# Performance work log

Hardware: AMD Instinct MI355X
Metric: run time of the kernel (lower is better)

Reference implementation:

```python
import jax, jax.numpy as jnp
import numpy as np

B, D, H, W = 16, 96, 96, 96
NUM_POINTS = 4096
THRESH = 0.5
CH = [3, 64, 128, 256, 512]   # shared-MLP channel progression (3 mlp layers + global_dim)
GROUPS = 8
EPS = 1e-5
HEAD_HIDDEN = 128


def setup_inputs() -> dict:
    key = jax.random.key(0)
    ks = jax.random.split(key, 8)
    inp = {"volume": jax.random.uniform(ks[0], (B, 1, D, H, W), jnp.float32)}
    for i in range(4):
        # Conv1d(kernel=1, no bias) weight (out, in); kaiming normal fan_out -> std=sqrt(2/out)
        inp[f"w{i+1}"] = jax.random.normal(ks[1 + i], (CH[i + 1], CH[i]), jnp.float32) * np.sqrt(2.0 / CH[i + 1]).astype(np.float32)
        inp[f"gn{i+1}_w"] = jnp.ones((CH[i + 1],), jnp.float32)
        inp[f"gn{i+1}_b"] = jnp.zeros((CH[i + 1],), jnp.float32)
    inp["fc1_w"] = jax.random.normal(ks[5], (HEAD_HIDDEN, CH[-1]), jnp.float32) * np.sqrt(2.0 / HEAD_HIDDEN).astype(np.float32)
    inp["fc1_b"] = jnp.zeros((HEAD_HIDDEN,), jnp.float32)
    inp["fc2_w"] = jax.random.normal(ks[6], (1, HEAD_HIDDEN), jnp.float32) * np.sqrt(2.0).astype(np.float32)
    inp["fc2_b"] = jnp.zeros((1,), jnp.float32)
    return inp


def volume_to_points(volume):
    """Batched, jit-safe version of volume_to_pointcloud (eval mode: linspace sampling)."""
    b, _, d, h, w = volume.shape
    mask = (volume[:, 0] > THRESH).reshape(b, -1)              # (B, D*H*W)
    n = mask.sum(axis=1)                                        # (B,) foreground counts
    # Stable argsort on ~mask puts foreground flat-indices first, in ascending order
    # == torch nonzero() ordering (row-major over D,H,W).
    order = jnp.argsort(jnp.logical_not(mask), axis=1, stable=True)  # (B, D*H*W)
    p = jnp.arange(NUM_POINTS)
    n_f = n.astype(jnp.float32)[:, None]
    # torch.linspace(0, n-1, P).long(): truncation toward zero
    lin = (p[None, :].astype(jnp.float32) * (n_f - 1.0) / (NUM_POINTS - 1)).astype(jnp.int32)
    lin = jnp.clip(lin, 0, jnp.maximum(n[:, None] - 1, 0))
    wrap = p[None, :] % jnp.maximum(n[:, None], 1)              # n < P fallback
    idx = jnp.where(n[:, None] >= NUM_POINTS, lin, wrap)        # (B, P)
    flat = jnp.take_along_axis(order, idx, axis=1)              # (B, P) flat voxel indices
    dd = flat // (h * w)
    hh = (flat // w) % h
    ww = flat % w
    coords = jnp.stack([dd, hh, ww], axis=1).astype(jnp.float32)  # (B, 3, P)
    scale = jnp.array([max(d - 1, 1), max(h - 1, 1), max(w - 1, 1)], jnp.float32)
    pts = coords / scale[None, :, None] * 2.0 - 1.0
    return jnp.where((n > 0)[:, None, None], pts, 0.0)


def group_norm(x, gamma, beta):
    b, c, npts = x.shape
    xg = x.reshape(b, GROUPS, c // GROUPS, npts)
    mu = xg.mean(axis=(2, 3), keepdims=True)
    var = xg.var(axis=(2, 3), keepdims=True)
    xn = ((xg - mu) * jax.lax.rsqrt(var + EPS)).reshape(b, c, npts)
    return xn * gamma[None, :, None] + beta[None, :, None]


def reference(volume, w1, gn1_w, gn1_b, w2, gn2_w, gn2_b, w3, gn3_w, gn3_b,
              w4, gn4_w, gn4_b, fc1_w, fc1_b, fc2_w, fc2_b):
    x = volume_to_points(volume)                                 # (B, 3, P)
    for cw, gw, gb in ((w1, gn1_w, gn1_b), (w2, gn2_w, gn2_b),
                       (w3, gn3_w, gn3_b), (w4, gn4_w, gn4_b)):
        x = jax.nn.relu(group_norm(jnp.einsum('oc,bcn->bon', cw, x), gw, gb))
    g = x.max(axis=2)                                            # (B, 512) global max-pool
    hdn = jax.nn.relu(g @ fc1_w.T + fc1_b)                       # dropout is identity in eval
    logits = (hdn @ fc2_w.T + fc2_b)[:, 0]                       # squeeze(-1) -> (B,)
    return logits
```

## Files before the change

### kernel.cpp

```cpp
#include <hip/hip_runtime.h>
#include <hip/hip_bf16.h>

#define NB 16
#define VOX 884736
#define NPTS 4096
#define CHUNK 1024
#define NCHUNK 864

typedef _Float16 f16x8 __attribute__((ext_vector_type(8)));
typedef _Float16 f16x4 __attribute__((ext_vector_type(4)));
typedef float f32x4 __attribute__((ext_vector_type(4)));


__global__ __launch_bounds__(256) void count_kernel(const float* __restrict__ vol,
                                                    int* __restrict__ counts,
                                                    unsigned long long* __restrict__ bits) {
    int blk = blockIdx.x;
    const float4* v4 = (const float4*)(vol + (size_t)blk * CHUNK);
    float4 v = v4[threadIdx.x];
    int nib = (v.x > 0.5f) | ((v.y > 0.5f) << 1) | ((v.z > 0.5f) << 2) | ((v.w > 0.5f) << 3);
    __shared__ unsigned char nibs[256];
    nibs[threadIdx.x] = (unsigned char)nib;
    int cnt = __popc(nib);
    for (int off = 32; off; off >>= 1) cnt += __shfl_down(cnt, off, 64);
    __shared__ int s[4];
    if ((threadIdx.x & 63) == 0) s[threadIdx.x >> 6] = cnt;
    __syncthreads();
    if (threadIdx.x < 16) {
        unsigned long long wd = 0;
        #pragma unroll
        for (int i = 0; i < 16; i++)
            wd |= (unsigned long long)nibs[threadIdx.x * 16 + i] << (4 * i);
        bits[(size_t)blk * 16 + threadIdx.x] = wd;
    }
    if (threadIdx.x == 0) counts[blk] = s[0] + s[1] + s[2] + s[3];
}

__global__ __launch_bounds__(1024) void scan_kernel(const int* __restrict__ counts,
                                                    int* __restrict__ prefix,
                                                    int* __restrict__ totals) {
    __shared__ int s[1024];
    int b = blockIdx.x, t = threadIdx.x;
    int v = (t < NCHUNK) ? counts[b * NCHUNK + t] : 0;
    s[t] = v;
    __syncthreads();
    for (int off = 1; off < 1024; off <<= 1) {
        int x = (t >= off) ? s[t - off] : 0;
        __syncthreads();
        s[t] += x;
        __syncthreads();
    }
    if (t < NCHUNK) prefix[b * NCHUNK + t] = s[t] - v;
    if (t == NCHUNK - 1) totals[b] = s[t];
}


__global__ __launch_bounds__(256) void points_kernel(const unsigned long long* __restrict__ bits,
                                                     const int* __restrict__ prefix,
                                                     const int* __restrict__ totals,
                                                     const float* __restrict__ w1,
                                                     float* __restrict__ pts,
                                                     float* __restrict__ pstat1) {
    int b = blockIdx.x >> 4;
    int pc = blockIdx.x & 15;
    int p = pc * 256 + threadIdx.x;
    __shared__ int spref[NCHUNK];
    __shared__ float sw1[192];
    for (int i = threadIdx.x; i < NCHUNK; i += 256) spref[i] = prefix[b * NCHUNK + i];
    if (threadIdx.x < 192) sw1[threadIdx.x] = w1[threadIdx.x];
    __syncthreads();
    int n = totals[b];
    float px = 0.f, py = 0.f, pz = 0.f;
    if (n > 0) {
        int k;
        if (n >= NPTS) {
            float t = (float)p * ((float)n - 1.0f);
            t = t / 4095.0f;
            k = (int)t;
            if (k > n - 1) k = n - 1;
            if (k < 0) k = 0;
        } else {
            k = p % n;
        }
        int lo = 0, hi = NCHUNK - 1;
        while (lo < hi) {
            int mid = (lo + hi + 1) >> 1;
            if (spref[mid] <= k) lo = mid; else hi = mid - 1;
        }
        int rr = k - spref[lo];
        const unsigned long long* wb = bits + ((size_t)b * NCHUNK + lo) * 16;
        unsigned long long chosen = 0;
        int wordidx = 0;
        bool found = false;
        #pragma unroll
        for (int w = 0; w < 16; w++) {
            unsigned long long m = wb[w];
            int pcnt = __popcll(m);
            bool take = (!found) && (rr < pcnt);
            if (take) { chosen = m; wordidx = w; found = true; }
            if (!found) rr -= pcnt;
        }
        int pos = 0;
        unsigned long long m64 = chosen;
        int c = __popcll(m64 & 0xFFFFFFFFull);
        if (rr >= c) { pos = 32; rr -= c; m64 >>= 32; }
        unsigned mm = (unsigned)m64;
        c = __popc(mm & 0xFFFFu); if (rr >= c) { pos += 16; rr -= c; mm >>= 16; }
        c = __popc(mm & 0xFFu);   if (rr >= c) { pos += 8;  rr -= c; mm >>= 8; }
        c = __popc(mm & 0xFu);    if (rr >= c) { pos += 4;  rr -= c; mm >>= 4; }
        c = __popc(mm & 0x3u);    if (rr >= c) { pos += 2;  rr -= c; mm >>= 2; }
        c = mm & 1u;              if (rr >= c) { pos += 1; }
        int flat = lo * CHUNK + wordidx * 64 + pos;
        int dd = flat / 9216;
        int rem = flat - dd * 9216;
        int hh = rem / 96;
        int ww = rem - hh * 96;
        px = (float)dd / 95.0f * 2.0f - 1.0f;
        py = (float)hh / 95.0f * 2.0f - 1.0f;
        pz = (float)ww / 95.0f * 2.0f - 1.0f;
    }
    pts[((size_t)b * 3 + 0) * NPTS + p] = px;
    pts[((size_t)b * 3 + 1) * NPTS + p] = py;
    pts[((size_t)b * 3 + 2) * NPTS + p] = pz;
    float s[8] = {}, q[8] = {};
    #pragma unroll
    for (int o = 0; o < 64; o++) {
        float a = sw1[o * 3 + 0] * px + sw1[o * 3 + 1] * py + sw1[o * 3 + 2] * pz;
        s[o >> 3] += a;
        q[o >> 3] += a * a;
    }
    __shared__ float red[4][8][2];
    int wv = threadIdx.x >> 6;
    #pragma unroll
    for (int g = 0; g < 8; g++) {
        float S = s[g], Q = q[g];
        for (int off = 32; off; off >>= 1) {
            S += __shfl_down(S, off, 64);
            Q += __shfl_down(Q, off, 64);
        }
        if ((threadIdx.x & 63) == 0) { red[wv][g][0] = S; red[wv][g][1] = Q; }
    }
    __syncthreads();
    if (threadIdx.x < 8) {
        int g = threadIdx.x;
        float S = red[0][g][0] + red[1][g][0] + red[2][g][0] + red[3][g][0];
        float Q = red[0][g][1] + red[1][g][1] + red[2][g][1] + red[3][g][1];
        float* d = pstat1 + (((size_t)(b * 8 + g)) * 16 + pc) * 2;
        d[0] = S; d[1] = Q;
    }
}

__global__ __launch_bounds__(64) void gn_finalize1(const float* __restrict__ pstat,
                                                   const float* __restrict__ gamma,
                                                   const float* __restrict__ beta,
                                                   float* __restrict__ scale,
                                                   float* __restrict__ shift) {
    int b = blockIdx.x >> 3, g = blockIdx.x & 7;
    const float* base = pstat + (size_t)(b * 8 + g) * 32;
    float S = 0.f, Q = 0.f;
    if (threadIdx.x < 16) { S = base[threadIdx.x * 2]; Q = base[threadIdx.x * 2 + 1]; }
    for (int off = 8; off; off >>= 1) {
        S += __shfl_down(S, off, 64);
        Q += __shfl_down(Q, off, 64);
    }
    __shared__ float ms[2];
    if (threadIdx.x == 0) {
        float inv = 1.0f / (8.0f * 4096.0f);
        float mu = S * inv;
        float var = Q * inv - mu * mu;
        if (var < 0.f) var = 0.f;
        ms[0] = mu; ms[1] = rsqrtf(var + 1e-5f);
    }
    __syncthreads();
    if (threadIdx.x < 8) {
        int c = g * 8 + threadIdx.x;
        float ga = gamma[c] * ms[1];
        scale[b * 64 + c] = ga;
        shift[b * 64 + c] = beta[c] - ms[0] * ga;
    }
}


__device__ inline void cast_chunk(const float* __restrict__ wf, _Float16* __restrict__ wh,
                                  int CIN, int t) {
    int lane = t & 63;
    int NCB = CIN / 32;
    int cb = (t >> 6) % NCB;
    int ob = t / (64 * NCB);
    int o = ob * 16 + (lane & 15);
    int c0 = cb * 32 + (lane >> 4) * 8;
    const float* src = wf + (size_t)o * CIN + c0;
    f16x8 v;
    #pragma unroll
    for (int e = 0; e < 8; e++) v[e] = (_Float16)src[e];
    *(f16x8*)(wh + (size_t)t * 8) = v;
}

__global__ __launch_bounds__(256) void cast_w_all(const float* __restrict__ w2,
                                                  const float* __restrict__ w3,
                                                  const float* __restrict__ w4,
                                                  _Float16* __restrict__ w2f,
                                                  _Float16* __restrict__ w3f,
                                                  _Float16* __restrict__ w4f) {
    int t = blockIdx.x * 256 + threadIdx.x;
    if (t < 1024) cast_chunk(w2, w2f, 64, t);
    else if (t < 1024 + 4096) cast_chunk(w3, w3f, 128, t - 1024);
    else if (t < 1024 + 4096 + 16384) cast_chunk(w4, w4f, 256, t - 5120);
}


template <int CIN, int COUT, bool POOL>
__device__ __forceinline__ void gemm_core(const _Float16* __restrict__ sl,
                                          const _Float16* __restrict__ wfrag,
                                          _Float16* __restrict__ yout,
                                          float* __restrict__ pstat,
                                          int b, int pblk, int tid) {
    constexpr int NCB = CIN / 32;
    constexpr int SLOT = CIN / 8 - 1;
    constexpr int OFW = COUT / 32;
    constexpr int COF = OFW > 4 ? 4 : OFW;
    constexpr int NCHK = OFW / COF;
    int wv = tid >> 6, lane = tid & 63, lr = lane & 15, lk = lane >> 4;
    int ph = wv & 1, oh = wv >> 1;
    int Pg = b * 64 + pblk;
    int pb32 = (Pg << 1) | ph;
    #pragma unroll
    for (int ck = 0; ck < NCHK; ck++) {
        f32x4 acc[2][COF] = {};
        for (int cb = 0; cb < NCB; cb++) {
            int ch = cb * 4 + lk;
            f16x8 af[2];
            #pragma unroll
            for (int pf = 0; pf < 2; pf++) {
                int p = ph * 32 + pf * 16 + lr;
                af[pf] = *(const f16x8*)(sl + p * CIN + ((ch ^ (p & SLOT)) << 3));
            }
            f16x8 bf[COF];
            #pragma unroll
            for (int i = 0; i < COF; i++) {
                int ofr = oh * OFW + ck * COF + i;
                bf[i] = *(const f16x8*)(wfrag + ((size_t)(ofr * NCB + cb) * 64 + lane) * 8);
            }
            #pragma unroll
            for (int pf = 0; pf < 2; pf++)
                #pragma unroll
                for (int i = 0; i < COF; i++)
                    acc[pf][i] = __builtin_amdgcn_mfma_f32_16x16x32_f16(af[pf], bf[i], acc[pf][i], 0, 0, 0);
        }
        #pragma unroll
        for (int i = 0; i < COF; i++) {
            int ofr = oh * OFW + ck * COF + i;
            if (!POOL) {
                _Float16* ytO = yout + ((size_t)Pg * (COUT / 64) + (ofr >> 2)) * 4096;
                #pragma unroll
                for (int pf = 0; pf < 2; pf++) {
                    f16x4 vv;
                    #pragma unroll
                    for (int j = 0; j < 4; j++) vv[j] = (_Float16)acc[pf][i][j];
                    *(f16x4*)(ytO + (((ofr & 3) * 4 + ph * 2 + pf) * 64 + lane) * 4) = vv;
                }
            }
            float S = 0.f, Q = 0.f, MX = -1e30f, MN = 1e30f;
            #pragma unroll
            for (int pf = 0; pf < 2; pf++)
                #pragma unroll
                for (int j = 0; j < 4; j++) {
                    float v = acc[pf][i][j];
                    S += v; Q += v * v;
                    if (POOL) { MX = fmaxf(MX, v); MN = fminf(MN, v); }
                }
            S += __shfl_xor(S, 16, 64); Q += __shfl_xor(Q, 16, 64);
            S += __shfl_xor(S, 32, 64); Q += __shfl_xor(Q, 32, 64);
            if (POOL) {
                MX = fmaxf(MX, __shfl_xor(MX, 16, 64)); MN = fminf(MN, __shfl_xor(MN, 16, 64));
                MX = fmaxf(MX, __shfl_xor(MX, 32, 64)); MN = fminf(MN, __shfl_xor(MN, 32, 64));
            }
            if (lk == 0) {
                int o = ofr * 16 + lr;
                if (POOL) {
                    *(float4*)(pstat + ((size_t)pb32 * COUT + o) * 4) = make_float4(S, Q, MX, MN);
                } else {
                    float* d = pstat + ((size_t)pb32 * COUT + o) * 2;
                    d[0] = S; d[1] = Q;
                }
            }
        }
    }
}


__global__ __launch_bounds__(256, 4) void fused_l2(const float* __restrict__ pts,
                                                   const float* __restrict__ w1,
                                                   const float* __restrict__ scale,
                                                   const float* __restrict__ shift,
                                                   const _Float16* __restrict__ wfrag,
                                                   _Float16* __restrict__ yout,
                                                   float* __restrict__ pstat) {
    __shared__ _Float16 sl[64 * 64];
    __shared__ float sw1[192], ssc[64], ssh[64];
    int b = blockIdx.y, pblk = blockIdx.x, tid = threadIdx.x;
    if (tid < 192) sw1[tid] = w1[tid];
    if (tid < 64) { ssc[tid] = scale[b * 64 + tid]; ssh[tid] = shift[b * 64 + tid]; }
    __syncthreads();
    {
        int p = tid >> 2, qo = (tid & 3) * 16;
        int pg = pblk * 64 + p;
        float x0 = pts[((size_t)b * 3 + 0) * NPTS + pg];
        float x1 = pts[((size_t)b * 3 + 1) * NPTS + pg];
        float x2 = pts[((size_t)b * 3 + 2) * NPTS + pg];
        #pragma unroll
        for (int e = 0; e < 16; e++) {
            int o = qo + e;
            float a = sw1[o * 3 + 0] * x0 + sw1[o * 3 + 1] * x1 + sw1[o * 3 + 2] * x2;
            float r = fmaxf(a * ssc[o] + ssh[o], 0.f);
            sl[p * 64 + (((o >> 3) ^ (p & 7)) << 3) + (o & 7)] = (_Float16)r;
        }
    }
    __syncthreads();
    gemm_core<64, 128, false>(sl, wfrag, yout, pstat, b, pblk, tid);
}


template <int CIN, int COUT, bool POOL>
__global__ __launch_bounds__(256, 4) void fused_layer(const _Float16* __restrict__ yprev,
                                                      const float* __restrict__ scale,
                                                      const float* __restrict__ shift,
                                                      const _Float16* __restrict__ wfrag,
                                                      _Float16* __restrict__ yout,
                                                      float* __restrict__ pstat) {
    constexpr int SLOT = CIN / 8 - 1;
    __shared__ _Float16 sl[64 * CIN];
    __shared__ float ssc[CIN], ssh[CIN];
    int b = blockIdx.y, pblk = blockIdx.x, tid = threadIdx.x;
    int Pg = b * 64 + pblk;
    for (int i = tid; i < CIN; i += 256) { ssc[i] = scale[b * CIN + i]; ssh[i] = shift[b * CIN + i]; }
    __syncthreads();
    const _Float16* yt = yprev + (size_t)Pg * 64 * CIN;
    constexpr int NCH4 = 64 * CIN / 4;
    for (int q = tid; q < NCH4; q += 256) {
        int lane = q & 63;
        int pf = (q >> 6) & 3;
        int ofi = (q >> 8) & 3;
        int Ob = q >> 10;
        int o = Ob * 64 + ofi * 16 + (lane & 15);
        int pbase = pf * 16 + (lane >> 4) * 4;
        f16x4 v = *(const f16x4*)(yt + (size_t)q * 4);
        float sc = ssc[o], sh = ssh[o];
        int ch = o >> 3;
        #pragma unroll
        for (int e = 0; e < 4; e++) {
            int p = pbase + e;
            float r = fmaxf((float)v[e] * sc + sh, 0.f);
            sl[p * CIN + ((ch ^ (p & SLOT)) << 3) + (o & 7)] = (_Float16)r;
        }
    }
    __syncthreads();
    gemm_core<CIN, COUT, POOL>(sl, wfrag, yout, pstat, b, pblk, tid);
}


template <int C>
__global__ __launch_bounds__(256) void gn_finalizeG(const float* __restrict__ pstat,
                                                    const float* __restrict__ gamma,
                                                    const float* __restrict__ beta,
                                                    float* __restrict__ scale,
                                                    float* __restrict__ shift) {
    constexpr int GS = C / 8;
    int b = blockIdx.x >> 3, g = blockIdx.x & 7;
    const float* base = pstat + (size_t)b * 128 * C * 2;
    float S = 0.f, Q = 0.f;
    for (int i = threadIdx.x; i < 128 * GS; i += 256) {
        int pb = i / GS;
        int c = g * GS + (i % GS);
        const float* d = base + ((size_t)pb * C + c) * 2;
        S += d[0]; Q += d[1];
    }
    for (int off = 32; off; off >>= 1) {
        S += __shfl_down(S, off, 64);
        Q += __shfl_down(Q, off, 64);
    }
    __shared__ float ss[8];
    if ((threadIdx.x & 63) == 0) {
        ss[(threadIdx.x >> 6) * 2] = S;
        ss[(threadIdx.x >> 6) * 2 + 1] = Q;
    }
    __syncthreads();
    __shared__ float ms[2];
    if (threadIdx.x == 0) {
        float St = ss[0] + ss[2] + ss[4] + ss[6];
        float Qt = ss[1] + ss[3] + ss[5] + ss[7];
        float inv = 1.0f / ((float)GS * 4096.0f);
        float mu = St * inv;
        float var = Qt * inv - mu * mu;
        if (var < 0.f) var = 0.f;
        ms[0] = mu; ms[1] = rsqrtf(var + 1e-5f);
    }
    __syncthreads();
    for (int i = threadIdx.x; i < GS; i += 256) {
        int c = g * GS + i;
        float ga = gamma[c] * ms[1];
        scale[(size_t)b * C + c] = ga;
        shift[(size_t)b * C + c] = beta[c] - ms[0] * ga;
    }
}


__global__ __launch_bounds__(64) void pool_final(const float* __restrict__ pstat4,
                                                 const float* __restrict__ gamma,
                                                 const float* __restrict__ beta,
                                                 float* __restrict__ g) {
    int b = blockIdx.x >> 3, gr = blockIdx.x & 7;
    int o = gr * 64 + threadIdx.x;
    float S = 0.f, Q = 0.f, MX = -1e30f, MN = 1e30f;
    for (int pb = 0; pb < 128; pb++) {
        float4 v = *(const float4*)(pstat4 + (((size_t)(b * 128 + pb)) * 512 + o) * 4);
        S += v.x; Q += v.y; MX = fmaxf(MX, v.z); MN = fminf(MN, v.w);
    }
    float St = S, Qt = Q;
    for (int off = 32; off; off >>= 1) {
        St += __shfl_xor(St, off, 64);
        Qt += __shfl_xor(Qt, off, 64);
    }
    float inv = 1.0f / (64.0f * 4096.0f);
    float mu = St * inv;
    float var = Qt * inv - mu * mu;
    if (var < 0.f) var = 0.f;
    float rstd = rsqrtf(var + 1e-5f);
    float sc = gamma[o] * rstd;
    float sh = beta[o] - mu * sc;
    float m = (sc >= 0.f ? MX : MN) * sc + sh;
    g[b * 512 + o] = fmaxf(m, 0.f);
}


__global__ __launch_bounds__(128) void head_kernel(const float* __restrict__ g,
                                                   const float* __restrict__ fc1w,
                                                   const float* __restrict__ fc1b,
                                                   const float* __restrict__ fc2w,
                                                   const float* __restrict__ fc2b,
                                                   float* __restrict__ out) {
    int b = blockIdx.x;
    int o = threadIdx.x;
    __shared__ float sg[512];
    for (int i = threadIdx.x; i < 512; i += 128) sg[i] = g[b * 512 + i];
    __syncthreads();
    float acc = fc1b[o];
    for (int c = 0; c < 512; c++) acc += sg[c] * fc1w[o * 512 + c];
    float h = fmaxf(acc, 0.f) * fc2w[o];
    for (int off = 32; off; off >>= 1) h += __shfl_down(h, off, 64);
    __shared__ float s2[2];
    if ((threadIdx.x & 63) == 0) s2[threadIdx.x >> 6] = h;
    __syncthreads();
    if (threadIdx.x == 0) out[b] = s2[0] + s2[1] + fc2b[0];
}


extern "C" void kernel_launch(void* const* d_in, const int* in_sizes, int n_in,
                              void* d_out, int out_size, void* d_ws, size_t ws_size,
                              hipStream_t stream) {
    const float* vol  = (const float*)d_in[0];
    const float* w1   = (const float*)d_in[1];
    const float* gn1w = (const float*)d_in[2];
    const float* gn1b = (const float*)d_in[3];
    const float* w2   = (const float*)d_in[4];
    const float* gn2w = (const float*)d_in[5];
    const float* gn2b = (const float*)d_in[6];
    const float* w3   = (const float*)d_in[7];
    const float* gn3w = (const float*)d_in[8];
    const float* gn3b = (const float*)d_in[9];
    const float* w4   = (const float*)d_in[10];
    const float* gn4w = (const float*)d_in[11];
    const float* gn4b = (const float*)d_in[12];
    const float* fc1w = (const float*)d_in[13];
    const float* fc1b = (const float*)d_in[14];
    const float* fc2w = (const float*)d_in[15];
    const float* fc2b = (const float*)d_in[16];
    float* out = (float*)d_out;

    char* ws = (char*)d_ws;
    size_t cur = 0;
    auto alloc = [&](size_t bytes) -> void* {
        cur = (cur + 255) & ~(size_t)255;
        void* p = ws + cur;
        cur += bytes;
        return p;
    };
    int*      counts  = (int*)alloc((size_t)NB * NCHUNK * 4);
    int*      prefix  = (int*)alloc((size_t)NB * NCHUNK * 4);
    int*      totals  = (int*)alloc(64);
    unsigned long long* bits = (unsigned long long*)alloc((size_t)NB * NCHUNK * 16 * 8);
    float*    pts     = (float*)alloc((size_t)NB * 3 * NPTS * 4);
    float*    gbuf    = (float*)alloc((size_t)NB * 512 * 4);
    float*    pstat1  = (float*)alloc((size_t)NB * 8 * 16 * 2 * 4);
    float*    pstatG  = (float*)alloc((size_t)NB * 128 * 256 * 2 * 4);
    float*    pstat4  = (float*)alloc((size_t)NB * 128 * 512 * 4 * 4);
    float*    scale   = (float*)alloc((size_t)NB * 512 * 4);
    float*    shift   = (float*)alloc((size_t)NB * 512 * 4);
    _Float16* w2f     = (_Float16*)alloc((size_t)128 * 64 * 2);
    _Float16* w3f     = (_Float16*)alloc((size_t)256 * 128 * 2);
    _Float16* w4f     = (_Float16*)alloc((size_t)512 * 256 * 2);
    _Float16* y2      = (_Float16*)alloc((size_t)NB * NPTS * 128 * 2);
    _Float16* y3      = (_Float16*)alloc((size_t)NB * NPTS * 256 * 2);

    count_kernel<<<dim3(NB * NCHUNK), dim3(256), 0, stream>>>(vol, counts, bits);
    scan_kernel<<<dim3(NB), dim3(1024), 0, stream>>>(counts, prefix, totals);
    points_kernel<<<dim3(NB * 16), dim3(256), 0, stream>>>(bits, prefix, totals, w1, pts, pstat1);

    cast_w_all<<<dim3(84), dim3(256), 0, stream>>>(w2, w3, w4, w2f, w3f, w4f);

    gn_finalize1<<<dim3(NB * 8), dim3(64), 0, stream>>>(pstat1, gn1w, gn1b, scale, shift);
    fused_l2<<<dim3(64, NB), dim3(256), 0, stream>>>(pts, w1, scale, shift, w2f, y2, pstatG);

    gn_finalizeG<128><<<dim3(NB * 8), dim3(256), 0, stream>>>(pstatG, gn2w, gn2b, scale, shift);
    fused_layer<128, 256, false><<<dim3(64, NB), dim3(256), 0, stream>>>(y2, scale, shift, w3f, y3, pstatG);

    gn_finalizeG<256><<<dim3(NB * 8), dim3(256), 0, stream>>>(pstatG, gn3w, gn3b, scale, shift);
    fused_layer<256, 512, true><<<dim3(64, NB), dim3(256), 0, stream>>>(y3, scale, shift, w4f, nullptr, pstat4);

    pool_final<<<dim3(NB * 8), dim3(64), 0, stream>>>(pstat4, gn4w, gn4b, gbuf);
    head_kernel<<<dim3(NB), dim3(128), 0, stream>>>(gbuf, fc1w, fc1b, fc2w, fc2b, out);
}
```

Baseline: 122.6 us.

## Overlap second-half tile staging with first-half MFMA and widen pool_final

In fused_layer, the second half of the input tile is loaded into registers up front. The GEMM over the first half of input channels runs while those loads are in flight, then the second half is normalised into LDS and the GEMM finishes. The aim is to hide global-load latency behind MFMA work. The LDS swizzle is widened to 16 slots for the larger channel counts to cut bank conflicts. pool_final now uses 256 threads that split the partial-block reduction four ways. These changes add register pressure and an extra barrier.

```diff
diff --git a/kernel.cpp b/kernel.cpp
--- a/kernel.cpp
+++ b/kernel.cpp
@@ -10,6 +10,13 @@
 typedef _Float16 f16x8 __attribute__((ext_vector_type(8)));
 typedef _Float16 f16x4 __attribute__((ext_vector_type(4)));
 typedef float f32x4 __attribute__((ext_vector_type(4)));
+
+template <int CIN>
+__device__ __forceinline__ int slotx(int ch, int p) {
+    if constexpr (CIN == 64)  return ch ^ (p & 7);
+    else if constexpr (CIN == 128) return ch ^ (p & 15);
+    else return (ch & 16) | ((ch & 15) ^ (p & 15));
+}
 
 
 __global__ __launch_bounds__(256) void count_kernel(const float* __restrict__ vol,
@@ -209,80 +216,78 @@
 }
 
 
-template <int CIN, int COUT, bool POOL>
-__device__ __forceinline__ void gemm_core(const _Float16* __restrict__ sl,
-                                          const _Float16* __restrict__ wfrag,
-                                          _Float16* __restrict__ yout,
-                                          float* __restrict__ pstat,
-                                          int b, int pblk, int tid) {
+template <int CIN, int COUT, int COF, int CBLO, int CBHI>
+__device__ __forceinline__ void gemm_range(const _Float16* __restrict__ sl,
+                                           const _Float16* __restrict__ wfrag,
+                                           f32x4 (&acc)[2][COF], int ck,
+                                           int ph, int oh, int lr, int lk, int lane) {
     constexpr int NCB = CIN / 32;
-    constexpr int SLOT = CIN / 8 - 1;
     constexpr int OFW = COUT / 32;
-    constexpr int COF = OFW > 4 ? 4 : OFW;
-    constexpr int NCHK = OFW / COF;
-    int wv = tid >> 6, lane = tid & 63, lr = lane & 15, lk = lane >> 4;
-    int ph = wv & 1, oh = wv >> 1;
-    int Pg = b * 64 + pblk;
-    int pb32 = (Pg << 1) | ph;
-    #pragma unroll
-    for (int ck = 0; ck < NCHK; ck++) {
-        f32x4 acc[2][COF] = {};
-        for (int cb = 0; cb < NCB; cb++) {
-            int ch = cb * 4 + lk;
-            f16x8 af[2];
+    #pragma unroll
+    for (int cb = CBLO; cb < CBHI; cb++) {
+        int ch = cb * 4 + lk;
+        f16x8 af[2];
+        #pragma unroll
+        for (int pf = 0; pf < 2; pf++) {
+            int p = ph * 32 + pf * 16 + lr;
+            af[pf] = *(const f16x8*)(sl + p * CIN + slotx<CIN>(ch, p) * 8);
+        }
+        f16x8 bf[COF];
+        #pragma unroll
+        for (int i = 0; i < COF; i++) {
+            int ofr = oh * OFW + ck * COF + i;
+            bf[i] = *(const f16x8*)(wfrag + ((size_t)(ofr * NCB + cb) * 64 + lane) * 8);
+        }
+        #pragma unroll
+        for (int pf = 0; pf < 2; pf++)
+            #pragma unroll
+            for (int i = 0; i < COF; i++)
+                acc[pf][i] = __builtin_amdgcn_mfma_f32_16x16x32_f16(af[pf], bf[i], acc[pf][i], 0, 0, 0);
+    }
+}
+
+template <int COUT, bool POOL, int COF>
+__device__ __forceinline__ void epilogue(f32x4 (&acc)[2][COF],
+                                         _Float16* __restrict__ yout,
+                                         float* __restrict__ pstat,
+                                         int Pg, int pb32, int ck,
+                                         int ph, int oh, int lr, int lk, int lane) {
+    constexpr int OFW = COUT / 32;
+    #pragma unroll
+    for (int i = 0; i < COF; i++) {
+        int ofr = oh * OFW + ck * COF + i;
+        if (!POOL) {
+            _Float16* ytO = yout + ((size_t)Pg * (COUT / 64) + (ofr >> 2)) * 4096;
             #pragma unroll
             for (int pf = 0; pf < 2; pf++) {
-                int p = ph * 32 + pf * 16 + lr;
-                af[pf] = *(const f16x8*)(sl + p * CIN + ((ch ^ (p & SLOT)) << 3));
+                f16x4 vv;
+                #pragma unroll
+                for (int j = 0; j < 4; j++) vv[j] = (_Float16)acc[pf][i][j];
+                *(f16x4*)(ytO + (((ofr & 3) * 4 + ph * 2 + pf) * 64 + lane) * 4) = vv;
             }
-            f16x8 bf[COF];
+        }
+        float S = 0.f, Q = 0.f, MX = -1e30f, MN = 1e30f;
+        #pragma unroll
+        for (int pf = 0; pf < 2; pf++)
             #pragma unroll
-            for (int i = 0; i < COF; i++) {
-                int ofr = oh * OFW + ck * COF + i;
-                bf[i] = *(const f16x8*)(wfrag + ((size_t)(ofr * NCB + cb) * 64 + lane) * 8);
+            for (int j = 0; j < 4; j++) {
+                float v = acc[pf][i][j];
+                S += v; Q += v * v;
+                if (POOL) { MX = fmaxf(MX, v); MN = fminf(MN, v); }
             }
-            #pragma unroll
-            for (int pf = 0; pf < 2; pf++)
-                #pragma unroll
-                for (int i = 0; i < COF; i++)
-                    acc[pf][i] = __builtin_amdgcn_mfma_f32_16x16x32_f16(af[pf], bf[i], acc[pf][i], 0, 0, 0);
-        }
-        #pragma unroll
-        for (int i = 0; i < COF; i++) {
-            int ofr = oh * OFW + ck * COF + i;
-            if (!POOL) {
-                _Float16* ytO = yout + ((size_t)Pg * (COUT / 64) + (ofr >> 2)) * 4096;
-                #pragma unroll
-                for (int pf = 0; pf < 2; pf++) {
-                    f16x4 vv;
-                    #pragma unroll
-                    for (int j = 0; j < 4; j++) vv[j] = (_Float16)acc[pf][i][j];
-                    *(f16x4*)(ytO + (((ofr & 3) * 4 + ph * 2 + pf) * 64 + lane) * 4) = vv;
-                }
-            }
-            float S = 0.f, Q = 0.f, MX = -1e30f, MN = 1e30f;
-            #pragma unroll
-            for (int pf = 0; pf < 2; pf++)
-                #pragma unroll
-                for (int j = 0; j < 4; j++) {
-                    float v = acc[pf][i][j];
-                    S += v; Q += v * v;
-                    if (POOL) { MX = fmaxf(MX, v); MN = fminf(MN, v); }
-                }
-            S += __shfl_xor(S, 16, 64); Q += __shfl_xor(Q, 16, 64);
-            S += __shfl_xor(S, 32, 64); Q += __shfl_xor(Q, 32, 64);
+        S += __shfl_xor(S, 16, 64); Q += __shfl_xor(Q, 16, 64);
+        S += __shfl_xor(S, 32, 64); Q += __shfl_xor(Q, 32, 64);
+        if (POOL) {
+            MX = fmaxf(MX, __shfl_xor(MX, 16, 64)); MN = fminf(MN, __shfl_xor(MN, 16, 64));
+            MX = fmaxf(MX, __shfl_xor(MX, 32, 64)); MN = fminf(MN, __shfl_xor(MN, 32, 64));
+        }
+        if (lk == 0) {
+            int o = ofr * 16 + lr;
             if (POOL) {
-                MX = fmaxf(MX, __shfl_xor(MX, 16, 64)); MN = fminf(MN, __shfl_xor(MN, 16, 64));
-                MX = fmaxf(MX, __shfl_xor(MX, 32, 64)); MN = fminf(MN, __shfl_xor(MN, 32, 64));
-            }
-            if (lk == 0) {
-                int o = ofr * 16 + lr;
-                if (POOL) {
-                    *(float4*)(pstat + ((size_t)pb32 * COUT + o) * 4) = make_float4(S, Q, MX, MN);
-                } else {
-                    float* d = pstat + ((size_t)pb32 * COUT + o) * 2;
-                    d[0] = S; d[1] = Q;
-                }
+                *(float4*)(pstat + ((size_t)pb32 * COUT + o) * 4) = make_float4(S, Q, MX, MN);
+            } else {
+                float* d = pstat + ((size_t)pb32 * COUT + o) * 2;
+                d[0] = S; d[1] = Q;
             }
         }
     }
@@ -313,11 +318,17 @@
             int o = qo + e;
             float a = sw1[o * 3 + 0] * x0 + sw1[o * 3 + 1] * x1 + sw1[o * 3 + 2] * x2;
             float r = fmaxf(a * ssc[o] + ssh[o], 0.f);
-            sl[p * 64 + (((o >> 3) ^ (p & 7)) << 3) + (o & 7)] = (_Float16)r;
-        }
-    }
-    __syncthreads();
-    gemm_core<64, 128, false>(sl, wfrag, yout, pstat, b, pblk, tid);
+            sl[p * 64 + slotx<64>(o >> 3, p) * 8 + (o & 7)] = (_Float16)r;
+        }
+    }
+    __syncthreads();
+    int wv = tid >> 6, lane = tid & 63, lr = lane & 15, lk = lane >> 4;
+    int ph = wv & 1, oh = wv >> 1;
+    int Pg = b * 64 + pblk;
+    int pb32 = (Pg << 1) | ph;
+    f32x4 acc[2][4] = {};
+    gemm_range<64, 128, 4, 0, 2>(sl, wfrag, acc, 0, ph, oh, lr, lk, lane);
+    epilogue<128, false, 4>(acc, yout, pstat, Pg, pb32, 0, ph, oh, lr, lk, lane);
 }
 
 
@@ -328,34 +339,72 @@
                                                       const _Float16* __restrict__ wfrag,
                                                       _Float16* __restrict__ yout,
                                                       float* __restrict__ pstat) {
-    constexpr int SLOT = CIN / 8 - 1;
+    constexpr int NCB = CIN / 32;
+    constexpr int OFW = COUT / 32;
+    constexpr int COF = 4;
+    constexpr int NCHK = OFW / COF;
+    constexpr int NCH4 = 64 * CIN / 4;
+    constexpr int HALF = NCH4 / 2;
+    constexpr int NREG = HALF / 256;
     __shared__ _Float16 sl[64 * CIN];
     __shared__ float ssc[CIN], ssh[CIN];
     int b = blockIdx.y, pblk = blockIdx.x, tid = threadIdx.x;
     int Pg = b * 64 + pblk;
     for (int i = tid; i < CIN; i += 256) { ssc[i] = scale[b * CIN + i]; ssh[i] = shift[b * CIN + i]; }
-    __syncthreads();
     const _Float16* yt = yprev + (size_t)Pg * 64 * CIN;
-    constexpr int NCH4 = 64 * CIN / 4;
-    for (int q = tid; q < NCH4; q += 256) {
-        int lane = q & 63;
-        int pf = (q >> 6) & 3;
-        int ofi = (q >> 8) & 3;
-        int Ob = q >> 10;
-        int o = Ob * 64 + ofi * 16 + (lane & 15);
-        int pbase = pf * 16 + (lane >> 4) * 4;
+    f16x4 rb[NREG];
+    #pragma unroll
+    for (int k = 0; k < NREG; k++)
+        rb[k] = *(const f16x4*)(yt + (size_t)(HALF + tid + k * 256) * 4);
+    __syncthreads();
+    #pragma unroll
+    for (int k = 0; k < NREG; k++) {
+        int q = tid + k * 256;
         f16x4 v = *(const f16x4*)(yt + (size_t)q * 4);
+        int ln = q & 63, pf = (q >> 6) & 3, ofi = (q >> 8) & 3, Ob = q >> 10;
+        int o = Ob * 64 + ofi * 16 + (ln & 15);
+        int pbase = pf * 16 + (ln >> 4) * 4;
         float sc = ssc[o], sh = ssh[o];
         int ch = o >> 3;
         #pragma unroll
         for (int e = 0; e < 4; e++) {
             int p = pbase + e;
             float r = fmaxf((float)v[e] * sc + sh, 0.f);
-            sl[p * CIN + ((ch ^ (p & SLOT)) << 3) + (o & 7)] = (_Float16)r;
-        }
-    }
-    __syncthreads();
-    gemm_core<CIN, COUT, POOL>(sl, wfrag, yout, pstat, b, pblk, tid);
+            sl[p * CIN + slotx<CIN>(ch, p) * 8 + (o & 7)] = (_Float16)r;
+        }
+    }
+    __syncthreads();
+    int wv = tid >> 6, lane = tid & 63, lr = lane & 15, lk = lane >> 4;
+    int ph = wv & 1, oh = wv >> 1;
+    int pb32 = (Pg << 1) | ph;
+    {
+        f32x4 acc[2][COF] = {};
+        gemm_range<CIN, COUT, COF, 0, NCB / 2>(sl, wfrag, acc, 0, ph, oh, lr, lk, lane);
+        #pragma unroll
+        for (int k = 0; k < NREG; k++) {
+            int q = HALF + tid + k * 256;
+            int ln = q & 63, pf = (q >> 6) & 3, ofi = (q >> 8) & 3, Ob = q >> 10;
+            int o = Ob * 64 + ofi * 16 + (ln & 15);
+            int pbase = pf * 16 + (ln >> 4) * 4;
+            float sc = ssc[o], sh = ssh[o];
+            int ch = o >> 3;
+            #pragma unroll
+            for (int e = 0; e < 4; e++) {
+                int p = pbase + e;
+                float r = fmaxf((float)rb[k][e] * sc + sh, 0.f);
+                sl[p * CIN + slotx<CIN>(ch, p) * 8 + (o & 7)] = (_Float16)r;
+            }
+        }
+        __syncthreads();
+        gemm_range<CIN, COUT, COF, NCB / 2, NCB>(sl, wfrag, acc, 0, ph, oh, lr, lk, lane);
+        epilogue<COUT, POOL, COF>(acc, yout, pstat, Pg, pb32, 0, ph, oh, lr, lk, lane);
+    }
+    #pragma unroll
+    for (int ck = 1; ck < NCHK; ck++) {
+        f32x4 acc[2][COF] = {};
+        gemm_range<CIN, COUT, COF, 0, NCB>(sl, wfrag, acc, ck, ph, oh, lr, lk, lane);
+        epilogue<COUT, POOL, COF>(acc, yout, pstat, Pg, pb32, ck, ph, oh, lr, lk, lane);
+    }
 }
 
 
@@ -405,31 +454,42 @@
 }
 
 
-__global__ __launch_bounds__(64) void pool_final(const float* __restrict__ pstat4,
-                                                 const float* __restrict__ gamma,
-                                                 const float* __restrict__ beta,
-                                                 float* __restrict__ g) {
+__global__ __launch_bounds__(256) void pool_final(const float* __restrict__ pstat4,
+                                                  const float* __restrict__ gamma,
+                                                  const float* __restrict__ beta,
+                                                  float* __restrict__ g) {
     int b = blockIdx.x >> 3, gr = blockIdx.x & 7;
-    int o = gr * 64 + threadIdx.x;
+    int ch = threadIdx.x & 63;
+    int pg = threadIdx.x >> 6;
+    int o = gr * 64 + ch;
     float S = 0.f, Q = 0.f, MX = -1e30f, MN = 1e30f;
-    for (int pb = 0; pb < 128; pb++) {
+    for (int pb = pg; pb < 128; pb += 4) {
         float4 v = *(const float4*)(pstat4 + (((size_t)(b * 128 + pb)) * 512 + o) * 4);
         S += v.x; Q += v.y; MX = fmaxf(MX, v.z); MN = fminf(MN, v.w);
     }
-    float St = S, Qt = Q;
-    for (int off = 32; off; off >>= 1) {
-        St += __shfl_xor(St, off, 64);
-        Qt += __shfl_xor(Qt, off, 64);
-    }
-    float inv = 1.0f / (64.0f * 4096.0f);
-    float mu = St * inv;
-    float var = Qt * inv - mu * mu;
-    if (var < 0.f) var = 0.f;
-    float rstd = rsqrtf(var + 1e-5f);
-    float sc = gamma[o] * rstd;
-    float sh = beta[o] - mu * sc;
-    float m = (sc >= 0.f ? MX : MN) * sc + sh;
-    g[b * 512 + o] = fmaxf(m, 0.f);
+    __shared__ float sS[4][64], sQ[4][64], sMX[4][64], sMN[4][64];
+    sS[pg][ch] = S; sQ[pg][ch] = Q; sMX[pg][ch] = MX; sMN[pg][ch] = MN;
+    __syncthreads();
+    if (threadIdx.x < 64) {
+        float Sc = sS[0][ch] + sS[1][ch] + sS[2][ch] + sS[3][ch];
+        float Qc = sQ[0][ch] + sQ[1][ch] + sQ[2][ch] + sQ[3][ch];
+        float MXc = fmaxf(fmaxf(sMX[0][ch], sMX[1][ch]), fmaxf(sMX[2][ch], sMX[3][ch]));
+        float MNc = fminf(fminf(sMN[0][ch], sMN[1][ch]), fminf(sMN[2][ch], sMN[3][ch]));
+        float St = Sc, Qt = Qc;
+        for (int off = 32; off; off >>= 1) {
+            St += __shfl_xor(St, off, 64);
+            Qt += __shfl_xor(Qt, off, 64);
+        }
+        float inv = 1.0f / (64.0f * 4096.0f);
+        float mu = St * inv;
+        float var = Qt * inv - mu * mu;
+        if (var < 0.f) var = 0.f;
+        float rstd = rsqrtf(var + 1e-5f);
+        float sc = gamma[o] * rstd;
+        float sh = beta[o] - mu * sc;
+        float m = (sc >= 0.f ? MXc : MNc) * sc + sh;
+        g[b * 512 + o] = fmaxf(m, 0.f);
+    }
 }
 
 
@@ -517,6 +577,6 @@
     gn_finalizeG<256><<<dim3(NB * 8), dim3(256), 0, stream>>>(pstatG, gn3w, gn3b, scale, shift);
     fused_layer<256, 512, true><<<dim3(64, NB), dim3(256), 0, stream>>>(y3, scale, shift, w4f, nullptr, pstat4);
 
-    pool_final<<<dim3(NB * 8), dim3(64), 0, stream>>>(pstat4, gn4w, gn4b, gbuf);
+    pool_final<<<dim3(NB * 8), dim3(256), 0, stream>>>(pstat4, gn4w, gn4b, gbuf);
     head_kernel<<<dim3(NB), dim3(128), 0, stream>>>(gbuf, fc1w, fc1b, fc2w, fc2b, out);
 }
```

After: 125.3 us. 1.02x slower.
